# Optimization experiments

Measured on AMD Instinct MI355X. Metric: run time of the kernel, lower is better.

The kernel has to match this reference:

```python
import jax, jax.numpy as jnp
import numpy as np

RADIUS = 0.1      # ball-query radius; also max_dist in collision_error
THRESH = 0.001    # collision threshold
NSAMPLE = 4       # neighbors per query point
EPS = 1e-7
LOSS_WEIGHT = 1.0


def _face_normals(verts, faces):
    # verts: (b, n_v, 3), faces: (b, n_f, 3) int -> unit face normals (b, n_f, 3)
    tri = jax.vmap(lambda V, F: V[F])(verts, faces)  # (b, n_f, 3verts, 3xyz)
    e1 = tri[:, :, 1] - tri[:, :, 0]
    e2 = tri[:, :, 2] - tri[:, :, 0]
    fn = jnp.cross(e1, e2)
    return fn / (jnp.linalg.norm(fn, axis=-1, keepdims=True) + EPS)


def _vertex_normals(faces, fn, n_v):
    # sparse v2f bmm equivalent: average incident face normals per vertex
    def scatter(F, N):
        idx = F.reshape(-1)                    # (3*n_f,) face->vertex ids
        vals = jnp.repeat(N, 3, axis=0)        # each face normal to its 3 verts
        s = jnp.zeros((n_v, 3), N.dtype).at[idx].add(vals)
        c = jnp.zeros((n_v, 1), N.dtype).at[idx].add(jnp.float32(1.0))
        return s / (c + EPS)
    return jax.vmap(scatter)(faces, fn)        # (b, n_v, 3)


def _ball_query(new_xyz, xyz, radius, nsample):
    # PointNet++ ball query: first `nsample` points of xyz within radius of each
    # new_xyz point; unfilled slots repeat the first hit (0 if no hits).
    d2 = jnp.sum((new_xyz[:, :, None, :] - xyz[:, None, :, :]) ** 2, axis=-1)  # (b, nq, nv)
    within = d2 < radius * radius
    c = jnp.cumsum(within.astype(jnp.int32), axis=-1)
    n_within = c[..., -1]
    first_idx = jnp.argmax(within, axis=-1)    # 0 when no hits (matches CUDA kernel)
    slots = []
    for j in range(nsample):
        idx_j = jnp.argmax(within & (c == j + 1), axis=-1)
        slots.append(jnp.where(n_within > j, idx_j, first_idx))
    return jnp.stack(slots, axis=-1)           # (b, nq, nsample)


def _collision_loss(pred, h_state, h_faces):
    faces = jnp.swapaxes(h_faces, 1, 2)                 # (b, n_f, 3)
    human_verts = jnp.swapaxes(h_state, 1, 2)[..., :3]  # (b, n_v, 3)
    n_v = human_verts.shape[1]

    fn = _face_normals(human_verts, faces)
    vn = _vertex_normals(faces, fn, n_v)                # (b, n_v, 3)

    idx = _ball_query(pred, human_verts, RADIUS, NSAMPLE)      # (b, nq, K)
    gxyz = jax.vmap(lambda V, I: V[I])(human_verts, idx)       # (b, nq, K, 3)
    gn = jax.vmap(lambda V, I: V[I])(vn, idx)                  # (b, nq, K, 3)

    diff = pred[:, :, None, :] - gxyz
    gn = gn / (jnp.linalg.norm(gn, axis=-1, keepdims=True) + EPS)
    dot = jnp.sum(diff * gn, axis=-1)                   # (b, nq, K)
    valid_dot = (dot - THRESH) * (dot >= -RADIUS)       # max_dist = radius
    mask = valid_dot < 0
    per_pt = jnp.sum(valid_dot * mask / (jnp.sum(mask, axis=-1, keepdims=True) + EPS), axis=-1) ** 2
    avg_mask = per_pt > 0
    loss = jnp.sum(per_pt)                              # reduction='sum', weight=None
    loss = loss / (jnp.sum(avg_mask) + EPS)
    return LOSS_WEIGHT * loss


def setup_inputs() -> dict:
    key = jax.random.key(0)
    k1, k2, k3, k4 = jax.random.split(key, 4)
    bs, n_pred, n_v, n_f, C = 2, 8192, 6890, 13776, 6
    pred = jax.random.uniform(k1, (bs, n_pred, 3), dtype=jnp.float32)
    label = jax.random.uniform(k2, (bs, n_pred, 3), dtype=jnp.float32)
    h_state = jax.random.uniform(k3, (bs, C, n_v), dtype=jnp.float32)
    h_faces = jax.random.randint(k4, (bs, 3, n_f), 0, n_v, dtype=jnp.int32)
    return {"pred": pred, "label": label, "h_state": h_state, "h_faces": h_faces}


def reference(pred, label, h_state, h_faces):
    # label is unused by collision_error (kept for signature fidelity)
    return _collision_loss(pred, h_state, h_faces)
```

## Files before the change

### kernel.cpp

```cpp
#include <hip/hip_runtime.h>
#include <cstdint>
#include <climits>

#define EPSF 1e-7f
#define NCELL 1000
#define RPAD 0.10002f


__device__ __forceinline__ int cell_of(float x, float y, float z) {
    int cx = min(max((int)(x * 10.0f), 0), 9);
    int cy = min(max((int)(y * 10.0f), 0), 9);
    int cz = min(max((int)(z * 10.0f), 0), 9);
    return (cx * 10 + cy) * 10 + cz;
}

__global__ void k12_build(const float* __restrict__ hs,
                          const int* __restrict__ hf,
                          float* __restrict__ svec,
                          float* __restrict__ scnt,
                          int* __restrict__ counts,
                          int* __restrict__ ctrl,
                          int* __restrict__ cellstart,
                          float4* __restrict__ spk,
                          int n_v, int n_f, int bs, int nfb) {
    __shared__ int cursor_l[NCELL];
    const int blk = blockIdx.x;

    if (blk < nfb) {
        int t = blk * blockDim.x + threadIdx.x;
        if (t < bs * n_f) {
            int b = t / n_f;
            int f = t - b * n_f;
            const int* fb = hf + (size_t)b * 3 * n_f;
            int i0 = fb[f];
            int i1 = fb[n_f + f];
            int i2 = fb[2 * n_f + f];
            const float* xs = hs + (size_t)b * 6 * n_v;
            const float* ys = xs + n_v;
            const float* zs = xs + 2 * n_v;
            float ax = xs[i0], ay = ys[i0], az = zs[i0];
            float bx = xs[i1], by = ys[i1], bz = zs[i1];
            float cx = xs[i2], cy = ys[i2], cz = zs[i2];
            float e1x = bx - ax, e1y = by - ay, e1z = bz - az;
            float e2x = cx - ax, e2y = cy - ay, e2z = cz - az;
            float fx = e1y * e2z - e1z * e2y;
            float fy = e1z * e2x - e1x * e2z;
            float fz = e1x * e2y - e1y * e2x;
            float nrm = sqrtf(fx * fx + fy * fy + fz * fz) + EPSF;
            fx /= nrm; fy /= nrm; fz /= nrm;
            float* sb = svec + (size_t)b * n_v * 3;
            float* cb = scnt + (size_t)b * n_v;
            atomicAdd(&sb[i0 * 3 + 0], fx);
            atomicAdd(&sb[i0 * 3 + 1], fy);
            atomicAdd(&sb[i0 * 3 + 2], fz);
            atomicAdd(&sb[i1 * 3 + 0], fx);
            atomicAdd(&sb[i1 * 3 + 1], fy);
            atomicAdd(&sb[i1 * 3 + 2], fz);
            atomicAdd(&sb[i2 * 3 + 0], fx);
            atomicAdd(&sb[i2 * 3 + 1], fy);
            atomicAdd(&sb[i2 * 3 + 2], fz);
            atomicAdd(&cb[i0], 1.0f);
            atomicAdd(&cb[i1], 1.0f);
            atomicAdd(&cb[i2], 1.0f);
        }
        if (t < bs * n_v) {
            int b = t / n_v;
            int v = t - b * n_v;
            const float* xs = hs + (size_t)b * 6 * n_v;
            float x = xs[v], y = xs[n_v + v], z = xs[2 * n_v + v];
            atomicAdd(&counts[b * NCELL + cell_of(x, y, z)], 1);
        }
        __syncthreads();
        if (threadIdx.x == 0) atomicAdd(&ctrl[0], 1);
        return;
    }

    const int batch = blk - nfb;
    if (threadIdx.x == 0) {
        while (atomicAdd(&ctrl[0], 0) < nfb) {  }
    }
    __syncthreads();

    if (threadIdx.x < 64) {
        int lane = threadIdx.x;
        int local[16];
        int mysum = 0;
        #pragma unroll
        for (int k = 0; k < 16; ++k) {
            int c = lane * 16 + k;
            int v = (c < NCELL) ? counts[batch * NCELL + c] : 0;
            local[k] = v;
            mysum += v;
        }
        int s = mysum;
        #pragma unroll
        for (int off = 1; off < 64; off <<= 1) {
            int n = __shfl_up(s, off);
            if (lane >= off) s += n;
        }
        int excl = s - mysum;
        #pragma unroll
        for (int k = 0; k < 16; ++k) {
            int c = lane * 16 + k;
            if (c < NCELL) {
                cellstart[batch * (NCELL + 1) + c] = excl;
                cursor_l[c] = excl;
                excl += local[k];
            }
        }
        if (lane == 63) cellstart[batch * (NCELL + 1) + NCELL] = s;
    }
    __syncthreads();
    const float* xs = hs + (size_t)batch * 6 * n_v;
    for (int v = threadIdx.x; v < n_v; v += blockDim.x) {
        float x = xs[v], y = xs[n_v + v], z = xs[2 * n_v + v];
        int cell = cell_of(x, y, z);
        int pos = atomicAdd(&cursor_l[cell], 1);
        spk[(size_t)batch * n_v + pos] = make_float4(x, y, z, __int_as_float(v));
    }
}

__global__ void k3_query(const float* __restrict__ pred,
                         const float* __restrict__ hs,
                         const float* __restrict__ svec,
                         const float* __restrict__ scnt,
                         const float4* __restrict__ spk,
                         const int* __restrict__ cellstart,
                         double* __restrict__ gsum,
                         float* __restrict__ gcnt,
                         int* __restrict__ ctrl,
                         float* __restrict__ out,
                         int n_v, int n_pred, int bs) {
    const int lane = threadIdx.x & 63;
    const int wave = threadIdx.x >> 6;
    const int sub = lane & 31;
    const int half = lane >> 5;
    const int qid = blockIdx.x * 8 + wave * 2 + half;
    const int nq = bs * n_pred;

    float per_pt = 0.0f;
    float is_pos = 0.0f;

    if (qid < nq) {
        const int b = qid / n_pred;
        const float4* sp = spk + (size_t)b * n_v;
        const int* csb = cellstart + b * (NCELL + 1);
        const float px = pred[(size_t)qid * 3 + 0];
        const float py = pred[(size_t)qid * 3 + 1];
        const float pz = pred[(size_t)qid * 3 + 2];

        int xlo = max(0, (int)floorf((px - RPAD) * 10.0f));
        int xhi = min(9, (int)floorf((px + RPAD) * 10.0f));
        int ylo = max(0, (int)floorf((py - RPAD) * 10.0f));
        int yhi = min(9, (int)floorf((py + RPAD) * 10.0f));
        int zlo = max(0, (int)floorf((pz - RPAD) * 10.0f));
        int zhi = min(9, (int)floorf((pz + RPAD) * 10.0f));

        int ip = min(sub, 8);
        int cxr = xlo + ip / 3;
        int cyr = ylo + ip % 3;
        bool validr = (cxr <= xhi) && (cyr <= yhi) && (sub < 9);
        int rowbase = (min(cxr, 9) * 10 + min(cyr, 9)) * 10;
        int rsv = csb[rowbase + zlo];
        int rev = csb[rowbase + zhi + 1];
        if (!validr) rev = rsv;

        unsigned PK[9];
        #pragma unroll
        for (int i = 0; i < 9; ++i) {
            unsigned rs = (unsigned)__shfl(rsv, i, 32);
            unsigned re = (unsigned)__shfl(rev, i, 32);
            PK[i] = (re << 16) | rs;
        }

        float4 c0[9];
        #pragma unroll
        for (int i = 0; i < 9; ++i) {
            int p = (int)(PK[i] & 0xffffu) + sub;
            c0[i] = sp[(p < (int)(PK[i] >> 16)) ? p : 0];
        }

        int l0 = INT_MAX, l1 = INT_MAX, l2 = INT_MAX, l3 = INT_MAX;
        #pragma unroll
        for (int i = 0; i < 9; ++i) {
            if ((int)(PK[i] & 0xffffu) + sub < (int)(PK[i] >> 16)) {
                float4 c4 = c0[i];
                float dx = px - c4.x;
                float dy = py - c4.y;
                float dz = pz - c4.z;
                float d2 = dx * dx + dy * dy + dz * dz;
                if (d2 < 0.01f) {
                    int vid = __float_as_int(c4.w);
                    if (vid < l3) {
                        if (vid < l1) {
                            if (vid < l0) { l3 = l2; l2 = l1; l1 = l0; l0 = vid; }
                            else          { l3 = l2; l2 = l1; l1 = vid; }
                        } else {
                            if (vid < l2) { l3 = l2; l2 = vid; }
                            else          { l3 = vid; }
                        }
                    }
                }
            }
        }
        #pragma unroll
        for (int i = 0; i < 9; ++i) {
            int re = (int)(PK[i] >> 16);
            for (int p = (int)(PK[i] & 0xffffu) + 32 + sub; p < re; p += 32) {
                float4 c4 = sp[p];
                float dx = px - c4.x;
                float dy = py - c4.y;
                float dz = pz - c4.z;
                float d2 = dx * dx + dy * dy + dz * dz;
                if (d2 < 0.01f) {
                    int vid = __float_as_int(c4.w);
                    if (vid < l3) {
                        if (vid < l1) {
                            if (vid < l0) { l3 = l2; l2 = l1; l1 = l0; l0 = vid; }
                            else          { l3 = l2; l2 = l1; l1 = vid; }
                        } else {
                            if (vid < l2) { l3 = l2; l2 = vid; }
                            else          { l3 = vid; }
                        }
                    }
                }
            }
        }

        #pragma unroll
        for (int off = 1; off < 32; off <<= 1) {
            int r0 = __shfl_xor(l3, off);
            int r1 = __shfl_xor(l2, off);
            int r2 = __shfl_xor(l1, off);
            int r3 = __shfl_xor(l0, off);
            int m0 = min(l0, r0);
            int m1 = min(l1, r1);
            int m2 = min(l2, r2);
            int m3 = min(l3, r3);
            int t0 = min(m0, m2), t2 = max(m0, m2);
            int t1 = min(m1, m3), t3 = max(m1, m3);
            l0 = min(t0, t1); l1 = max(t0, t1);
            l2 = min(t2, t3); l3 = max(t2, t3);
        }

        int id0 = (l0 == INT_MAX) ? 0 : l0;
        int id1 = (l1 == INT_MAX) ? id0 : l1;
        int id2 = (l2 == INT_MAX) ? id0 : l2;
        int id3 = (l3 == INT_MAX) ? id0 : l3;
        int ids[4] = {id0, id1, id2, id3};

        const float* xs = hs + (size_t)b * 6 * n_v;
        const float* ysv = xs + n_v;
        const float* zsv = xs + 2 * n_v;
        const float* svb = svec + (size_t)b * n_v * 3;
        const float* scb = scnt + (size_t)b * n_v;

        float vd[4];
        float cm = 0.0f;
        #pragma unroll
        for (int j = 0; j < 4; ++j) {
            int id = ids[j];
            float cc = scb[id] + EPSF;
            float vx = svb[id * 3 + 0] / cc;
            float vy = svb[id * 3 + 1] / cc;
            float vz = svb[id * 3 + 2] / cc;
            float nrm = sqrtf(vx * vx + vy * vy + vz * vz) + EPSF;
            float njx = vx / nrm, njy = vy / nrm, njz = vz / nrm;
            float dx = px - xs[id];
            float dy = py - ysv[id];
            float dz = pz - zsv[id];
            float dot = dx * njx + dy * njy + dz * njz;
            float w = (dot >= -0.1f) ? 1.0f : 0.0f;
            float v = (dot - 0.001f) * w;
            bool msk = v < 0.0f;
            vd[j] = msk ? v : 0.0f;
            cm += msk ? 1.0f : 0.0f;
        }
        float s = ((vd[0] + vd[1]) + vd[2]) + vd[3];
        float a = s / (cm + EPSF);
        per_pt = a * a;
        is_pos = (per_pt > 0.0f) ? 1.0f : 0.0f;
    }

    __shared__ float ls[8];
    __shared__ float lc[8];
    __shared__ int lastflag;
    if (sub == 0) {
        int slot = wave * 2 + half;
        ls[slot] = per_pt;
        lc[slot] = is_pos;
    }
    __syncthreads();
    if (threadIdx.x == 0) {
        double ssum = 0.0;
        float csum = 0.0f;
        #pragma unroll
        for (int k = 0; k < 8; ++k) {
            ssum += (double)ls[k];
            csum += lc[k];
        }
        double o1 = atomicAdd(&gsum[blockIdx.x & 63], ssum);
        float  o2 = atomicAdd(&gcnt[blockIdx.x & 63], csum);
        float oo = (float)o1 + o2;
        asm volatile("" : : "v"(oo) : "memory");
        int old = atomicAdd(&ctrl[1], 1);
        lastflag = (old == (int)gridDim.x - 1) ? 1 : 0;
    }
    __syncthreads();
    if (lastflag) {
        if (threadIdx.x < 64) {
            double s = atomicAdd(&gsum[threadIdx.x], 0.0);
            double c = (double)atomicAdd(&gcnt[threadIdx.x], 0.0f);
            #pragma unroll
            for (int off = 32; off > 0; off >>= 1) {
                s += __shfl_down(s, off);
                c += __shfl_down(c, off);
            }
            if (threadIdx.x == 0) out[0] = (float)(s / (c + 1e-7));
        }
    }
}

extern "C" void kernel_launch(void* const* d_in, const int* in_sizes, int n_in,
                              void* d_out, int out_size, void* d_ws, size_t ws_size,
                              hipStream_t stream) {
    const float* pred    = (const float*)d_in[0];
    const float* h_state = (const float*)d_in[2];
    const int*   h_faces = (const int*)d_in[3];
    float* out = (float*)d_out;

    const int bs = 2;
    const int n_pred = in_sizes[0] / (bs * 3);
    const int n_v    = in_sizes[2] / (bs * 6);
    const int n_f    = in_sizes[3] / (bs * 3);
    const int nq = bs * n_pred;
    const int nblk = (nq + 7) / 8;
    const int nfb  = (bs * n_f + 511) / 512;

    size_t o_svec    = 0;
    size_t o_scnt    = o_svec + (size_t)bs * n_v * 3;
    size_t o_counts  = o_scnt + (size_t)bs * n_v;
    size_t o_ctrl    = o_counts + (size_t)bs * NCELL;
    size_t o_gsum    = (o_ctrl + 2 + 1) & ~(size_t)1;
    size_t o_gcnt    = o_gsum + 2 * 64;
    size_t o_zeroend = (o_gcnt + 64 + 3) & ~(size_t)3;
    size_t o_cs      = o_zeroend;
    size_t o_spk     = (o_cs + (size_t)bs * (NCELL + 1) + 3) & ~(size_t)3;

    float* base = (float*)d_ws;
    float*  svec      = base + o_svec;
    float*  scnt      = base + o_scnt;
    int*    counts    = (int*)(base + o_counts);
    int*    ctrl      = (int*)(base + o_ctrl);
    double* gsum      = (double*)(base + o_gsum);
    float*  gcnt      = base + o_gcnt;
    int*    cellstart = (int*)(base + o_cs);
    float4* spk       = (float4*)(base + o_spk);

    hipMemsetAsync(d_ws, 0, o_zeroend * sizeof(float), stream);

    k12_build<<<nfb + bs, 512, 0, stream>>>(
        h_state, h_faces, svec, scnt, counts, ctrl, cellstart, spk,
        n_v, n_f, bs, nfb);

    k3_query<<<nblk, 256, 0, stream>>>(
        pred, h_state, svec, scnt, spk, cellstart, gsum, gcnt, ctrl, out,
        n_v, n_pred, bs);
}
```

Baseline: 122.6 us.

## Build cell histogram in shared memory and replace last-block reduction with finalize kernel

```diff
diff --git a/kernel.cpp b/kernel.cpp
--- a/kernel.cpp
+++ b/kernel.cpp
@@ -14,16 +14,14 @@
     return (cx * 10 + cy) * 10 + cz;
 }
 
-__global__ void k12_build(const float* __restrict__ hs,
-                          const int* __restrict__ hf,
-                          float* __restrict__ svec,
-                          float* __restrict__ scnt,
-                          int* __restrict__ counts,
-                          int* __restrict__ ctrl,
-                          int* __restrict__ cellstart,
-                          float4* __restrict__ spk,
-                          int n_v, int n_f, int bs, int nfb) {
-    __shared__ int cursor_l[NCELL];
+__global__ void k_ab(const float* __restrict__ hs,
+                     const int* __restrict__ hf,
+                     float* __restrict__ svec,
+                     float* __restrict__ scnt,
+                     int* __restrict__ cellstart,
+                     float4* __restrict__ spk,
+                     int n_v, int n_f, int bs, int nfb) {
+    __shared__ int hist[NCELL];
     const int blk = blockIdx.x;
 
     if (blk < nfb) {
@@ -63,21 +61,17 @@
             atomicAdd(&cb[i1], 1.0f);
             atomicAdd(&cb[i2], 1.0f);
         }
-        if (t < bs * n_v) {
-            int b = t / n_v;
-            int v = t - b * n_v;
-            const float* xs = hs + (size_t)b * 6 * n_v;
-            float x = xs[v], y = xs[n_v + v], z = xs[2 * n_v + v];
-            atomicAdd(&counts[b * NCELL + cell_of(x, y, z)], 1);
-        }
-        __syncthreads();
-        if (threadIdx.x == 0) atomicAdd(&ctrl[0], 1);
         return;
     }
 
     const int batch = blk - nfb;
-    if (threadIdx.x == 0) {
-        while (atomicAdd(&ctrl[0], 0) < nfb) {  }
+    const float* xs = hs + (size_t)batch * 6 * n_v;
+
+    for (int c = threadIdx.x; c < NCELL; c += blockDim.x) hist[c] = 0;
+    __syncthreads();
+    for (int v = threadIdx.x; v < n_v; v += blockDim.x) {
+        float x = xs[v], y = xs[n_v + v], z = xs[2 * n_v + v];
+        atomicAdd(&hist[cell_of(x, y, z)], 1);
     }
     __syncthreads();
 
@@ -88,7 +82,7 @@
         #pragma unroll
         for (int k = 0; k < 16; ++k) {
             int c = lane * 16 + k;
-            int v = (c < NCELL) ? counts[batch * NCELL + c] : 0;
+            int v = (c < NCELL) ? hist[c] : 0;
             local[k] = v;
             mysum += v;
         }
@@ -104,32 +98,31 @@
             int c = lane * 16 + k;
             if (c < NCELL) {
                 cellstart[batch * (NCELL + 1) + c] = excl;
-                cursor_l[c] = excl;
+                hist[c] = excl;
                 excl += local[k];
             }
         }
         if (lane == 63) cellstart[batch * (NCELL + 1) + NCELL] = s;
     }
     __syncthreads();
-    const float* xs = hs + (size_t)batch * 6 * n_v;
+
     for (int v = threadIdx.x; v < n_v; v += blockDim.x) {
         float x = xs[v], y = xs[n_v + v], z = xs[2 * n_v + v];
         int cell = cell_of(x, y, z);
-        int pos = atomicAdd(&cursor_l[cell], 1);
+        int pos = atomicAdd(&hist[cell], 1);
         spk[(size_t)batch * n_v + pos] = make_float4(x, y, z, __int_as_float(v));
     }
 }
 
-__global__ void k3_query(const float* __restrict__ pred,
+__global__ __launch_bounds__(256, 8) void k3_query(
+                         const float* __restrict__ pred,
                          const float* __restrict__ hs,
                          const float* __restrict__ svec,
                          const float* __restrict__ scnt,
                          const float4* __restrict__ spk,
                          const int* __restrict__ cellstart,
-                         double* __restrict__ gsum,
-                         float* __restrict__ gcnt,
-                         int* __restrict__ ctrl,
-                         float* __restrict__ out,
+                         double* __restrict__ partial,
+                         float* __restrict__ pcnt,
                          int n_v, int n_pred, int bs) {
     const int lane = threadIdx.x & 63;
     const int wave = threadIdx.x >> 6;
@@ -284,7 +277,6 @@
 
     __shared__ float ls[8];
     __shared__ float lc[8];
-    __shared__ int lastflag;
     if (sub == 0) {
         int slot = wave * 2 + half;
         ls[slot] = per_pt;
@@ -299,25 +291,34 @@
             ssum += (double)ls[k];
             csum += lc[k];
         }
-        double o1 = atomicAdd(&gsum[blockIdx.x & 63], ssum);
-        float  o2 = atomicAdd(&gcnt[blockIdx.x & 63], csum);
-        float oo = (float)o1 + o2;
-        asm volatile("" : : "v"(oo) : "memory");
-        int old = atomicAdd(&ctrl[1], 1);
-        lastflag = (old == (int)gridDim.x - 1) ? 1 : 0;
-    }
-    __syncthreads();
-    if (lastflag) {
-        if (threadIdx.x < 64) {
-            double s = atomicAdd(&gsum[threadIdx.x], 0.0);
-            double c = (double)atomicAdd(&gcnt[threadIdx.x], 0.0f);
-            #pragma unroll
-            for (int off = 32; off > 0; off >>= 1) {
-                s += __shfl_down(s, off);
-                c += __shfl_down(c, off);
-            }
-            if (threadIdx.x == 0) out[0] = (float)(s / (c + 1e-7));
-        }
+        partial[blockIdx.x] = ssum;
+        pcnt[blockIdx.x] = csum;
+    }
+}
+
+__global__ void finalize_kernel(const double* __restrict__ partial,
+                                const float* __restrict__ pcnt,
+                                int n, float* __restrict__ out) {
+    double s = 0.0, c = 0.0;
+    for (int i = threadIdx.x; i < n; i += blockDim.x) {
+        s += partial[i];
+        c += (double)pcnt[i];
+    }
+    #pragma unroll
+    for (int off = 32; off > 0; off >>= 1) {
+        s += __shfl_down(s, off);
+        c += __shfl_down(c, off);
+    }
+    __shared__ double ws_s[4];
+    __shared__ double ws_c[4];
+    int wave = threadIdx.x >> 6;
+    int lane = threadIdx.x & 63;
+    if (lane == 0) { ws_s[wave] = s; ws_c[wave] = c; }
+    __syncthreads();
+    if (threadIdx.x == 0) {
+        double S = ws_s[0] + ws_s[1] + ws_s[2] + ws_s[3];
+        double C = ws_c[0] + ws_c[1] + ws_c[2] + ws_c[3];
+        out[0] = (float)(S / (C + 1e-7));
     }
 }
 
@@ -335,35 +336,32 @@
     const int n_f    = in_sizes[3] / (bs * 3);
     const int nq = bs * n_pred;
     const int nblk = (nq + 7) / 8;
-    const int nfb  = (bs * n_f + 511) / 512;
+    const int nfb  = (bs * n_f + 1023) / 1024;
 
     size_t o_svec    = 0;
     size_t o_scnt    = o_svec + (size_t)bs * n_v * 3;
-    size_t o_counts  = o_scnt + (size_t)bs * n_v;
-    size_t o_ctrl    = o_counts + (size_t)bs * NCELL;
-    size_t o_gsum    = (o_ctrl + 2 + 1) & ~(size_t)1;
-    size_t o_gcnt    = o_gsum + 2 * 64;
-    size_t o_zeroend = (o_gcnt + 64 + 3) & ~(size_t)3;
+    size_t o_zeroend = (o_scnt + (size_t)bs * n_v + 3) & ~(size_t)3;
     size_t o_cs      = o_zeroend;
-    size_t o_spk     = (o_cs + (size_t)bs * (NCELL + 1) + 3) & ~(size_t)3;
+    size_t o_partial = (o_cs + (size_t)bs * (NCELL + 1) + 1) & ~(size_t)1;
+    size_t o_pcnt    = o_partial + 2 * (size_t)nblk;
+    size_t o_spk     = (o_pcnt + (size_t)nblk + 3) & ~(size_t)3;
 
     float* base = (float*)d_ws;
     float*  svec      = base + o_svec;
     float*  scnt      = base + o_scnt;
-    int*    counts    = (int*)(base + o_counts);
-    int*    ctrl      = (int*)(base + o_ctrl);
-    double* gsum      = (double*)(base + o_gsum);
-    float*  gcnt      = base + o_gcnt;
     int*    cellstart = (int*)(base + o_cs);
+    double* partial   = (double*)(base + o_partial);
+    float*  pcnt      = base + o_pcnt;
     float4* spk       = (float4*)(base + o_spk);
 
     hipMemsetAsync(d_ws, 0, o_zeroend * sizeof(float), stream);
 
-    k12_build<<<nfb + bs, 512, 0, stream>>>(
-        h_state, h_faces, svec, scnt, counts, ctrl, cellstart, spk,
-        n_v, n_f, bs, nfb);
+    k_ab<<<nfb + bs, 1024, 0, stream>>>(
+        h_state, h_faces, svec, scnt, cellstart, spk, n_v, n_f, bs, nfb);
 
     k3_query<<<nblk, 256, 0, stream>>>(
-        pred, h_state, svec, scnt, spk, cellstart, gsum, gcnt, ctrl, out,
+        pred, h_state, svec, scnt, spk, cellstart, partial, pcnt,
         n_v, n_pred, bs);
-}
+
+    finalize_kernel<<<1, 256, 0, stream>>>(partial, pcnt, nblk, out);
+}
```

Result: faster. 112.0 us (-8.6%).
